# Kernel optimization log

Hardware: AMD Instinct MI355X
Metric: run time of the kernel (lower is better)

## Reference

```python
import jax, jax.numpy as jnp
import numpy as np

NUM_LAYERS = 2      # args.num_layers
EPS = 1e-6          # poincare_to_lorentz eps
NORM_CLIP = 1.0     # exp_map norm_control clip
N, K, F, D = 30000, 32, 256, 128


def _normalize_lorentz(h):
    # project onto hyperboloid: time = sqrt(1 + |space|^2)
    sp = h[:, 1:]
    t = jnp.sqrt(1.0 + jnp.sum(sp * sp, axis=-1, keepdims=True))
    return jnp.concatenate([t, sp], axis=-1)


def _exp_map_zero(v):
    # tangent vector at origin has zero time component (normalize_tan with x=0)
    sp = v[:, 1:]
    ldv = jnp.sum(sp * sp, axis=-1, keepdims=True)          # Lorentz norm^2 of (0, sp)
    nd = jnp.sqrt(jnp.clip(ldv + 1e-9, 1e-10, None))
    t = jnp.minimum(nd, NORM_CLIP)                           # norm_control
    time = jnp.cosh(t)
    space = jnp.sinh(t) * sp / nd
    return _normalize_lorentz(jnp.concatenate([time, space], axis=-1))


def _hyperbolic_mean(nbr, w):
    # nbr: [N, K, D] Lorentz points; w: [N, K] neighbor weights
    k = nbr[..., 1:] / nbr[..., :1]                          # h2k: Klein model
    kn = jnp.clip(jnp.sum(k * k, axis=-1, keepdims=True), 0.0, 0.9)
    lam = w[..., None] / jnp.sqrt(1.0 - kn)                  # weighted Lorentz factors
    k_mean = jnp.sum(lam * k, axis=1) / jnp.sum(lam, axis=1)  # [N, D-1]
    # k2h: Klein -> hyperboloid
    kn2 = jnp.minimum(jnp.sum(k_mean * k_mean, axis=-1, keepdims=True), 0.9)
    ones = jnp.ones((k_mean.shape[0], 1), k_mean.dtype)
    return jnp.concatenate([ones, k_mean], axis=-1) / jnp.sqrt(1.0 - kn2)


def _lorentz_activation(h):
    # lorentz -> poincare, SELU, poincare -> lorentz (c = 1)
    p = h[:, 1:] / (h[:, :1] + 1.0)
    p = jax.nn.selu(p)
    pn = jnp.sum(p * p, axis=-1, keepdims=True)
    return jnp.concatenate([1.0 + pn, 2.0 * p], axis=-1) / (1.0 - pn + EPS)


def setup_inputs() -> dict:
    key = jax.random.key(0)
    k1, k2, k3, k4, k5 = jax.random.split(key, 5)
    x = jax.random.normal(k1, (N, F), dtype=jnp.float32)
    adj = jax.random.randint(k2, (N, K), 0, N, dtype=jnp.int32)
    w = jax.random.uniform(k3, (N, K), dtype=jnp.float32)
    lin_W = jax.random.normal(k4, (F, D), dtype=jnp.float32) / np.sqrt(F)
    lin_b = jnp.zeros((D,), dtype=jnp.float32)
    M, _ = jnp.linalg.qr(jax.random.normal(k5, (D - 1, D - 1), dtype=jnp.float32))  # orthogonal init
    return {"x": x, "adj": adj, "w": w, "lin_W": lin_W, "lin_b": lin_b, "M": M}


def reference(x, adj, w, lin_W, lin_b, M):
    h = jax.nn.selu(x @ lin_W + lin_b)          # Euclidean projection + activation
    h = _exp_map_zero(h)                        # lift to hyperboloid
    d = h.shape[-1]
    # retrieve_params: block-diag [[1,0],[0,M]] Lorentz rotation (tie_weight -> shared)
    lw = jnp.zeros((d, d), h.dtype).at[0, 0].set(1.0).at[1:, 1:].set(M)
    for _ in range(NUM_LAYERS):
        msg = h @ lw                             # Stiefel transform
        nbr = msg[adj]                           # [N, K, D] neighbor gather
        h = _hyperbolic_mean(nbr, w)             # Klein weighted mean
        h = _lorentz_activation(h)               # SELU in Poincare model
        h = _normalize_lorentz(h)                # re-project onto hyperboloid
    return h
```

## Files before the change

### kernel.cpp

```cpp
#include <hip/hip_runtime.h>
#include <hip/hip_fp16.h>
#include <math.h>

#define NN 30000
#define KK 32
#define FF 256
#define DD 128
#define NB16 1875
#define SA 268

typedef _Float16 f16x8 __attribute__((ext_vector_type(8)));
typedef _Float16 f16x2 __attribute__((ext_vector_type(2)));
typedef float f32x4v __attribute__((ext_vector_type(4)));

__device__ __forceinline__ float seluf(float x) {
    const float scale = 1.0507009873554804934193349852946f;
    const float alpha = 1.6732632423543772848170429916717f;
    return x > 0.f ? scale * x : scale * alpha * expm1f(x);
}

__device__ __forceinline__ float waveReduceSum(float v) {
#pragma unroll
    for (int m = 1; m < 64; m <<= 1) v += __shfl_xor(v, m, 64);
    return v;
}

__global__ __launch_bounds__(256) void k_prep(
    const float* __restrict__ W, const float* __restrict__ M,
    _Float16* __restrict__ Wt, _Float16* __restrict__ Lt)
{
    const int b = blockIdx.x, t = threadIdx.x;
    if (b < 128) {
        Wt[b * FF + t] = (_Float16)W[t * DD + b];
    } else if (t < 128) {
        const int c = b - 128, k = t;
        const float v = (k == 0 && c == 0) ? 1.f
                      : ((k >= 1 && c >= 1) ? M[(k - 1) * 127 + (c - 1)] : 0.f);
        Lt[c * DD + k] = (_Float16)v;
    }
}

__global__ __launch_bounds__(256) void k_lin_exp_msg(
    const float* __restrict__ x, const _Float16* __restrict__ Wt,
    const float* __restrict__ b, const _Float16* __restrict__ Lt,
    __half* __restrict__ table)
{
    __shared__ _Float16 as_[16][SA];
    __shared__ _Float16 hhi[16][SA];
    __shared__ _Float16 hlo[16][SA];
    __shared__ float red[4][16];
    __shared__ float m0s[16];
    const int wv_ = threadIdx.x >> 6;
    const int lane = threadIdx.x & 63;
    const int g = lane >> 4, c16 = lane & 15;
    const int baseRow = blockIdx.x * 16;
    const int nb = wv_ * 2;
    const int arow = baseRow + c16;

    {
        const float4* xp = (const float4*)(x + (size_t)arow * FF);
#pragma unroll
        for (int i = 0; i < 2; ++i) {
            const int ks = wv_ * 2 + i;
            const float4 f0 = xp[ks * 8 + g * 2];
            const float4 f1 = xp[ks * 8 + g * 2 + 1];
            const float q[8] = {f0.x, f0.y, f0.z, f0.w, f1.x, f1.y, f1.z, f1.w};
            f16x8 a;
#pragma unroll
            for (int j = 0; j < 8; ++j) a[j] = (_Float16)q[j];
            *(f16x8*)&as_[c16][ks * 32 + g * 8] = a;
        }
    }
    __syncthreads();

    f16x8 bw0[8], bw1[8];
#pragma unroll
    for (int ks = 0; ks < 8; ++ks) {
        bw0[ks] = *(const f16x8*)(Wt + (size_t)((nb + 0) * 16 + c16) * FF + ks * 32 + g * 8);
        bw1[ks] = *(const f16x8*)(Wt + (size_t)((nb + 1) * 16 + c16) * FF + ks * 32 + g * 8);
    }
    f16x8 af[8];
#pragma unroll
    for (int ks = 0; ks < 8; ++ks)
        af[ks] = *(const f16x8*)&as_[c16][ks * 32 + g * 8];

    f32x4v acc[2];
    acc[0] = acc[1] = f32x4v{0.f, 0.f, 0.f, 0.f};
#pragma unroll
    for (int ks = 0; ks < 8; ++ks) {
        acc[0] = __builtin_amdgcn_mfma_f32_16x16x32_f16(af[ks], bw0[ks], acc[0], 0, 0, 0);
        acc[1] = __builtin_amdgcn_mfma_f32_16x16x32_f16(af[ks], bw1[ks], acc[1], 0, 0, 0);
    }

    float bias[2];
#pragma unroll
    for (int n = 0; n < 2; ++n) bias[n] = b[(nb + n) * 16 + c16];

    float vv[4][2];
#pragma unroll
    for (int r = 0; r < 4; ++r) {
        float part = 0.f;
#pragma unroll
        for (int n = 0; n < 2; ++n) {
            vv[r][n] = seluf(acc[n][r] + bias[n]);
            float sq = vv[r][n] * vv[r][n];
            if (wv_ == 0 && n == 0 && c16 == 0) sq = 0.f;
            part += sq;
        }
#pragma unroll
        for (int m = 1; m < 16; m <<= 1) part += __shfl_xor(part, m, 64);
        if (c16 == 0) red[wv_][4 * g + r] = part;
    }
    __syncthreads();
#pragma unroll
    for (int r = 0; r < 4; ++r) {
        const int lrow = 4 * g + r;
        const float ldv = red[0][lrow] + red[1][lrow] + red[2][lrow] + red[3][lrow];
        const float nd = sqrtf(fmaxf(ldv + 1e-9f, 1e-10f));
        const float t  = fminf(nd, 1.0f);
        const float sc = sinhf(t) / nd;
        const float tm = sqrtf(1.f + sc * sc * ldv);
#pragma unroll
        for (int n = 0; n < 2; ++n) {
            const int col = (nb + n) * 16 + c16;
            const float o = (wv_ == 0 && n == 0 && c16 == 0) ? tm : sc * vv[r][n];
            const _Float16 hi = (_Float16)o;
            hhi[lrow][col] = hi;
            hlo[lrow][col] = (_Float16)(o - (float)hi);
        }
    }
    __syncthreads();

    f16x8 bl0[4], bl1[4];
#pragma unroll
    for (int ks = 0; ks < 4; ++ks) {
        bl0[ks] = *(const f16x8*)(Lt + (size_t)((nb + 0) * 16 + c16) * DD + ks * 32 + g * 8);
        bl1[ks] = *(const f16x8*)(Lt + (size_t)((nb + 1) * 16 + c16) * DD + ks * 32 + g * 8);
    }
    f16x8 mh[4], ml[4];
#pragma unroll
    for (int ks = 0; ks < 4; ++ks) {
        mh[ks] = *(const f16x8*)&hhi[c16][ks * 32 + g * 8];
        ml[ks] = *(const f16x8*)&hlo[c16][ks * 32 + g * 8];
    }
    acc[0] = acc[1] = f32x4v{0.f, 0.f, 0.f, 0.f};
#pragma unroll
    for (int ks = 0; ks < 4; ++ks) {
        acc[0] = __builtin_amdgcn_mfma_f32_16x16x32_f16(mh[ks], bl0[ks], acc[0], 0, 0, 0);
        acc[0] = __builtin_amdgcn_mfma_f32_16x16x32_f16(ml[ks], bl0[ks], acc[0], 0, 0, 0);
        acc[1] = __builtin_amdgcn_mfma_f32_16x16x32_f16(mh[ks], bl1[ks], acc[1], 0, 0, 0);
        acc[1] = __builtin_amdgcn_mfma_f32_16x16x32_f16(ml[ks], bl1[ks], acc[1], 0, 0, 0);
    }

#pragma unroll
    for (int r = 0; r < 4; ++r) {
        float part = 0.f;
#pragma unroll
        for (int n = 0; n < 2; ++n) {
            float sq = acc[n][r] * acc[n][r];
            if (wv_ == 0 && n == 0 && c16 == 0) sq = 0.f;
            part += sq;
        }
#pragma unroll
        for (int m = 1; m < 16; m <<= 1) part += __shfl_xor(part, m, 64);
        if (c16 == 0) red[wv_][4 * g + r] = part;
        if (wv_ == 0 && c16 == 0) m0s[4 * g + r] = acc[0][r];
    }
    __syncthreads();
#pragma unroll
    for (int r = 0; r < 4; ++r) {
        const int lrow = 4 * g + r;
        const int row = baseRow + lrow;
        const float rn = 1.f / m0s[lrow];
        const float sum2 = red[0][lrow] + red[1][lrow] + red[2][lrow] + red[3][lrow];
        float kn = sum2 * rn * rn;
        kn = fminf(fmaxf(kn, 0.f), 0.9f);
        const float fh = 1.f / sqrtf(1.f - kn);
#pragma unroll
        for (int n = 0; n < 2; ++n) {
            const float val = (wv_ == 0 && n == 0 && c16 == 0) ? fh : acc[n][r] * rn;
            table[(size_t)row * DD + (nb + n) * 16 + c16] = __float2half(val);
        }
    }
}

__global__ __launch_bounds__(256) void k_layer_msg(
    const __half* __restrict__ tin, const int* __restrict__ adj,
    const float* __restrict__ w, const _Float16* __restrict__ Lt,
    __half* __restrict__ tout)
{
    __shared__ _Float16 hhi[16][SA];
    __shared__ _Float16 hlo[16][SA];
    __shared__ float red[4][16];
    __shared__ float m0s[16];
    const int wv_ = threadIdx.x >> 6;
    const int lane = threadIdx.x & 63;
    const int g = lane >> 4, c16 = lane & 15;
    const int baseNode = blockIdx.x * 16;

#pragma unroll
    for (int q = 0; q < 4; ++q) {
        const int node = baseNode + wv_ * 4 + q;
        const int   av = adj[node * KK + (lane & 31)];
        const float wvv = w[node * KK + (lane & 31)];

        unsigned int vbits[32];
#pragma unroll
        for (int j = 0; j < KK; ++j) {
            const int idx = __shfl(av, j, 64);
            vbits[j] = *(const unsigned int*)(tin + (size_t)idx * DD + lane * 2);
        }
        const float f = __half2float(tin[(size_t)av * DD]);
        const float lam = wvv * f;
        float ls = lam;
#pragma unroll
        for (int m = 1; m < 32; m <<= 1) ls += __shfl_xor(ls, m, 64);

        float km0 = 0.f, km1 = 0.f;
#pragma unroll
        for (int j = 0; j < KK; ++j) {
            const float cj = __shfl(lam, j, 64);
            const __half2 hh = *(const __half2*)&vbits[j];
            const float2 v = __half22float2(hh);
            km0 = fmaf(cj, v.x, km0);
            km1 = fmaf(cj, v.y, km1);
        }
        const float rl = 1.f / ls;
        const float m0 = km0 * rl;
        const float m1 = km1 * rl;
        float c2 = (lane ? m0 * m0 : 0.f) + m1 * m1;
        const float kn2 = fminf(waveReduceSum(c2), 0.9f);
        const float invs = 1.f / sqrtf(1.f - kn2);
        const float pd = invs + 1.f;
        const float p0 = lane ? seluf(m0 * invs / pd) : 0.f;
        const float p1 = seluf(m1 * invs / pd);
        float pc = p0 * p0 + p1 * p1;
        const float pn = waveReduceSum(pc);
        const float rdn = 1.f / (1.f - pn + 1e-6f);
        const float tm = sqrtf(1.f + 4.f * pn * rdn * rdn);
        const float ox = lane ? 2.f * p0 * rdn : tm;
        const float oy = 2.f * p1 * rdn;
        const int lrow = wv_ * 4 + q;
        const _Float16 hx = (_Float16)ox;
        const _Float16 hy = (_Float16)oy;
        f16x2 hi2, lo2;
        hi2[0] = hx; hi2[1] = hy;
        lo2[0] = (_Float16)(ox - (float)hx);
        lo2[1] = (_Float16)(oy - (float)hy);
        *(f16x2*)&hhi[lrow][2 * lane] = hi2;
        *(f16x2*)&hlo[lrow][2 * lane] = lo2;
    }
    __syncthreads();

    const int nb = wv_ * 2;
    f16x8 bl0[4], bl1[4];
#pragma unroll
    for (int ks = 0; ks < 4; ++ks) {
        bl0[ks] = *(const f16x8*)(Lt + (size_t)((nb + 0) * 16 + c16) * DD + ks * 32 + g * 8);
        bl1[ks] = *(const f16x8*)(Lt + (size_t)((nb + 1) * 16 + c16) * DD + ks * 32 + g * 8);
    }
    f16x8 mh[4], ml[4];
#pragma unroll
    for (int ks = 0; ks < 4; ++ks) {
        mh[ks] = *(const f16x8*)&hhi[c16][ks * 32 + g * 8];
        ml[ks] = *(const f16x8*)&hlo[c16][ks * 32 + g * 8];
    }
    f32x4v acc[2];
    acc[0] = acc[1] = f32x4v{0.f, 0.f, 0.f, 0.f};
#pragma unroll
    for (int ks = 0; ks < 4; ++ks) {
        acc[0] = __builtin_amdgcn_mfma_f32_16x16x32_f16(mh[ks], bl0[ks], acc[0], 0, 0, 0);
        acc[0] = __builtin_amdgcn_mfma_f32_16x16x32_f16(ml[ks], bl0[ks], acc[0], 0, 0, 0);
        acc[1] = __builtin_amdgcn_mfma_f32_16x16x32_f16(mh[ks], bl1[ks], acc[1], 0, 0, 0);
        acc[1] = __builtin_amdgcn_mfma_f32_16x16x32_f16(ml[ks], bl1[ks], acc[1], 0, 0, 0);
    }

#pragma unroll
    for (int r = 0; r < 4; ++r) {
        float part = 0.f;
#pragma unroll
        for (int n = 0; n < 2; ++n) {
            float sq = acc[n][r] * acc[n][r];
            if (wv_ == 0 && n == 0 && c16 == 0) sq = 0.f;
            part += sq;
        }
#pragma unroll
        for (int m = 1; m < 16; m <<= 1) part += __shfl_xor(part, m, 64);
        if (c16 == 0) red[wv_][4 * g + r] = part;
        if (wv_ == 0 && c16 == 0) m0s[4 * g + r] = acc[0][r];
    }
    __syncthreads();
#pragma unroll
    for (int r = 0; r < 4; ++r) {
        const int lrow = 4 * g + r;
        const int row = baseNode + lrow;
        const float rn = 1.f / m0s[lrow];
        const float sum2 = red[0][lrow] + red[1][lrow] + red[2][lrow] + red[3][lrow];
        float kn = sum2 * rn * rn;
        kn = fminf(fmaxf(kn, 0.f), 0.9f);
        const float fh = 1.f / sqrtf(1.f - kn);
#pragma unroll
        for (int n = 0; n < 2; ++n) {
            const float val = (wv_ == 0 && n == 0 && c16 == 0) ? fh : acc[n][r] * rn;
            tout[(size_t)row * DD + (nb + n) * 16 + c16] = __float2half(val);
        }
    }
}

__global__ __launch_bounds__(256) void k_layer(
    const __half* __restrict__ table, const int* __restrict__ adj,
    const float* __restrict__ w, float* __restrict__ out)
{
    const int wave = threadIdx.x >> 6;
    const int lane = threadIdx.x & 63;
    const int node = blockIdx.x * 4 + wave;

    const int   av = adj[node * KK + (lane & 31)];
    const float wv = w[node * KK + (lane & 31)];

    unsigned int vbits[32];
#pragma unroll
    for (int j = 0; j < KK; ++j) {
        const int idx = __shfl(av, j, 64);
        vbits[j] = *(const unsigned int*)(table + (size_t)idx * DD + lane * 2);
    }

    const float f  = __half2float(table[(size_t)av * DD]);
    const float lam = wv * f;
    float ls = lam;
#pragma unroll
    for (int m = 1; m < 32; m <<= 1) ls += __shfl_xor(ls, m, 64);

    float km0 = 0.f, km1 = 0.f;
#pragma unroll
    for (int j = 0; j < KK; ++j) {
        const float cj = __shfl(lam, j, 64);
        const __half2 hh = *(const __half2*)&vbits[j];
        const float2 v = __half22float2(hh);
        km0 = fmaf(cj, v.x, km0);
        km1 = fmaf(cj, v.y, km1);
    }
    const float rl = 1.f / ls;
    const float m0 = km0 * rl;
    const float m1 = km1 * rl;
    float c2 = (lane ? m0 * m0 : 0.f) + m1 * m1;
    const float kn2 = fminf(waveReduceSum(c2), 0.9f);
    const float invs = 1.f / sqrtf(1.f - kn2);
    const float pd = invs + 1.f;
    const float p0 = lane ? seluf(m0 * invs / pd) : 0.f;
    const float p1 = seluf(m1 * invs / pd);
    float pc = p0 * p0 + p1 * p1;
    const float pn = waveReduceSum(pc);
    const float rdn = 1.f / (1.f - pn + 1e-6f);
    const float tm = sqrtf(1.f + 4.f * pn * rdn * rdn);
    float2 o;
    o.x = lane ? 2.f * p0 * rdn : tm;
    o.y = 2.f * p1 * rdn;
    *(float2*)(out + (size_t)node * DD + lane * 2) = o;
}

extern "C" void kernel_launch(void* const* d_in, const int* in_sizes, int n_in,
                              void* d_out, int out_size, void* d_ws, size_t ws_size,
                              hipStream_t stream) {
    const float* x     = (const float*)d_in[0];
    const int*   adj   = (const int*)d_in[1];
    const float* w     = (const float*)d_in[2];
    const float* lin_W = (const float*)d_in[3];
    const float* lin_b = (const float*)d_in[4];
    const float* M     = (const float*)d_in[5];
    float*  out   = (float*)d_out;
    char*   ws    = (char*)d_ws;
    __half*   table0 = (__half*)ws;
    __half*   table1 = (__half*)(ws + 7680000);
    _Float16* Wt     = (_Float16*)(ws + 15360000);
    _Float16* Lt     = (_Float16*)(ws + 15425536);

    k_prep<<<256, 256, 0, stream>>>(lin_W, M, Wt, Lt);
    k_lin_exp_msg<<<NB16, 256, 0, stream>>>(x, Wt, lin_b, Lt, table0);
    k_layer_msg<<<NB16, 256, 0, stream>>>(table0, adj, w, Lt, table1);
    k_layer<<<NN / 4, 256, 0, stream>>>(table1, adj, w, out);
}
```

Measured before the change: 113.0 us.

## Use 16 waves per block in layer-msg kernel, one node per wave

The layer message kernel now launches 1024 threads per block, so each of 16 waves gathers and aggregates one node in parallel instead of four waves each looping over four nodes. The following small GEMM is split so 8 waves each compute one 16-column tile, with reductions widened to 8 partials. Separately, the first kernel reuses the hhi shared buffer for its input staging, which shrinks its LDS footprint. The aim is more memory-level parallelism on the gather and higher occupancy. The cost is half the waves idling during the GEMM phase and more register pressure under the new launch bounds.

```diff
diff --git a/kernel.cpp b/kernel.cpp
--- a/kernel.cpp
+++ b/kernel.cpp
@@ -45,7 +45,6 @@
     const float* __restrict__ b, const _Float16* __restrict__ Lt,
     __half* __restrict__ table)
 {
-    __shared__ _Float16 as_[16][SA];
     __shared__ _Float16 hhi[16][SA];
     __shared__ _Float16 hlo[16][SA];
     __shared__ float red[4][16];
@@ -68,7 +67,7 @@
             f16x8 a;
 #pragma unroll
             for (int j = 0; j < 8; ++j) a[j] = (_Float16)q[j];
-            *(f16x8*)&as_[c16][ks * 32 + g * 8] = a;
+            *(f16x8*)&hhi[c16][ks * 32 + g * 8] = a;
         }
     }
     __syncthreads();
@@ -82,7 +81,7 @@
     f16x8 af[8];
 #pragma unroll
     for (int ks = 0; ks < 8; ++ks)
-        af[ks] = *(const f16x8*)&as_[c16][ks * 32 + g * 8];
+        af[ks] = *(const f16x8*)&hhi[c16][ks * 32 + g * 8];
 
     f32x4v acc[2];
     acc[0] = acc[1] = f32x4v{0.f, 0.f, 0.f, 0.f};
@@ -184,23 +183,22 @@
     }
 }
 
-__global__ __launch_bounds__(256) void k_layer_msg(
+__global__ __launch_bounds__(1024, 8) void k_layer_msg(
     const __half* __restrict__ tin, const int* __restrict__ adj,
     const float* __restrict__ w, const _Float16* __restrict__ Lt,
     __half* __restrict__ tout)
 {
     __shared__ _Float16 hhi[16][SA];
     __shared__ _Float16 hlo[16][SA];
-    __shared__ float red[4][16];
+    __shared__ float red[8][16];
     __shared__ float m0s[16];
     const int wv_ = threadIdx.x >> 6;
     const int lane = threadIdx.x & 63;
     const int g = lane >> 4, c16 = lane & 15;
     const int baseNode = blockIdx.x * 16;
 
-#pragma unroll
-    for (int q = 0; q < 4; ++q) {
-        const int node = baseNode + wv_ * 4 + q;
+    {
+        const int node = baseNode + wv_;
         const int   av = adj[node * KK + (lane & 31)];
         const float wvv = w[node * KK + (lane & 31)];
 
@@ -240,69 +238,60 @@
         const float tm = sqrtf(1.f + 4.f * pn * rdn * rdn);
         const float ox = lane ? 2.f * p0 * rdn : tm;
         const float oy = 2.f * p1 * rdn;
-        const int lrow = wv_ * 4 + q;
         const _Float16 hx = (_Float16)ox;
         const _Float16 hy = (_Float16)oy;
         f16x2 hi2, lo2;
         hi2[0] = hx; hi2[1] = hy;
         lo2[0] = (_Float16)(ox - (float)hx);
         lo2[1] = (_Float16)(oy - (float)hy);
-        *(f16x2*)&hhi[lrow][2 * lane] = hi2;
-        *(f16x2*)&hlo[lrow][2 * lane] = lo2;
-    }
-    __syncthreads();
-
-    const int nb = wv_ * 2;
-    f16x8 bl0[4], bl1[4];
-#pragma unroll
-    for (int ks = 0; ks < 4; ++ks) {
-        bl0[ks] = *(const f16x8*)(Lt + (size_t)((nb + 0) * 16 + c16) * DD + ks * 32 + g * 8);
-        bl1[ks] = *(const f16x8*)(Lt + (size_t)((nb + 1) * 16 + c16) * DD + ks * 32 + g * 8);
-    }
-    f16x8 mh[4], ml[4];
-#pragma unroll
-    for (int ks = 0; ks < 4; ++ks) {
-        mh[ks] = *(const f16x8*)&hhi[c16][ks * 32 + g * 8];
-        ml[ks] = *(const f16x8*)&hlo[c16][ks * 32 + g * 8];
-    }
-    f32x4v acc[2];
-    acc[0] = acc[1] = f32x4v{0.f, 0.f, 0.f, 0.f};
-#pragma unroll
-    for (int ks = 0; ks < 4; ++ks) {
-        acc[0] = __builtin_amdgcn_mfma_f32_16x16x32_f16(mh[ks], bl0[ks], acc[0], 0, 0, 0);
-        acc[0] = __builtin_amdgcn_mfma_f32_16x16x32_f16(ml[ks], bl0[ks], acc[0], 0, 0, 0);
-        acc[1] = __builtin_amdgcn_mfma_f32_16x16x32_f16(mh[ks], bl1[ks], acc[1], 0, 0, 0);
-        acc[1] = __builtin_amdgcn_mfma_f32_16x16x32_f16(ml[ks], bl1[ks], acc[1], 0, 0, 0);
-    }
-
-#pragma unroll
-    for (int r = 0; r < 4; ++r) {
-        float part = 0.f;
-#pragma unroll
-        for (int n = 0; n < 2; ++n) {
-            float sq = acc[n][r] * acc[n][r];
-            if (wv_ == 0 && n == 0 && c16 == 0) sq = 0.f;
-            part += sq;
-        }
-#pragma unroll
-        for (int m = 1; m < 16; m <<= 1) part += __shfl_xor(part, m, 64);
-        if (c16 == 0) red[wv_][4 * g + r] = part;
-        if (wv_ == 0 && c16 == 0) m0s[4 * g + r] = acc[0][r];
-    }
-    __syncthreads();
-#pragma unroll
-    for (int r = 0; r < 4; ++r) {
-        const int lrow = 4 * g + r;
-        const int row = baseNode + lrow;
-        const float rn = 1.f / m0s[lrow];
-        const float sum2 = red[0][lrow] + red[1][lrow] + red[2][lrow] + red[3][lrow];
-        float kn = sum2 * rn * rn;
-        kn = fminf(fmaxf(kn, 0.f), 0.9f);
-        const float fh = 1.f / sqrtf(1.f - kn);
-#pragma unroll
-        for (int n = 0; n < 2; ++n) {
-            const float val = (wv_ == 0 && n == 0 && c16 == 0) ? fh : acc[n][r] * rn;
-            tout[(size_t)row * DD + (nb + n) * 16 + c16] = __float2half(val);
+        *(f16x2*)&hhi[wv_][2 * lane] = hi2;
+        *(f16x2*)&hlo[wv_][2 * lane] = lo2;
+    }
+    __syncthreads();
+
+    f32x4v acc = f32x4v{0.f, 0.f, 0.f, 0.f};
+    const int nb = wv_;
+    if (wv_ < 8) {
+        f16x8 bl[4];
+#pragma unroll
+        for (int ks = 0; ks < 4; ++ks)
+            bl[ks] = *(const f16x8*)(Lt + (size_t)(nb * 16 + c16) * DD + ks * 32 + g * 8);
+        f16x8 mh[4], ml[4];
+#pragma unroll
+        for (int ks = 0; ks < 4; ++ks) {
+            mh[ks] = *(const f16x8*)&hhi[c16][ks * 32 + g * 8];
+            ml[ks] = *(const f16x8*)&hlo[c16][ks * 32 + g * 8];
+        }
+#pragma unroll
+        for (int ks = 0; ks < 4; ++ks) {
+            acc = __builtin_amdgcn_mfma_f32_16x16x32_f16(mh[ks], bl[ks], acc, 0, 0, 0);
+            acc = __builtin_amdgcn_mfma_f32_16x16x32_f16(ml[ks], bl[ks], acc, 0, 0, 0);
+        }
+#pragma unroll
+        for (int r = 0; r < 4; ++r) {
+            float sq = acc[r] * acc[r];
+            if (nb == 0 && c16 == 0) sq = 0.f;
+#pragma unroll
+            for (int m = 1; m < 16; m <<= 1) sq += __shfl_xor(sq, m, 64);
+            if (c16 == 0) red[wv_][4 * g + r] = sq;
+            if (nb == 0 && c16 == 0) m0s[4 * g + r] = acc[r];
+        }
+    }
+    __syncthreads();
+    if (wv_ < 8) {
+#pragma unroll
+        for (int r = 0; r < 4; ++r) {
+            const int lrow = 4 * g + r;
+            const int row = baseNode + lrow;
+            const float rn = 1.f / m0s[lrow];
+            float sum2 = 0.f;
+#pragma unroll
+            for (int i = 0; i < 8; ++i) sum2 += red[i][lrow];
+            float kn = sum2 * rn * rn;
+            kn = fminf(fmaxf(kn, 0.f), 0.9f);
+            const float fh = 1.f / sqrtf(1.f - kn);
+            const float val = (nb == 0 && c16 == 0) ? fh : acc[r] * rn;
+            tout[(size_t)row * DD + nb * 16 + c16] = __float2half(val);
         }
     }
 }
@@ -377,6 +366,6 @@
 
     k_prep<<<256, 256, 0, stream>>>(lin_W, M, Wt, Lt);
     k_lin_exp_msg<<<NB16, 256, 0, stream>>>(x, Wt, lin_b, Lt, table0);
-    k_layer_msg<<<NB16, 256, 0, stream>>>(table0, adj, w, Lt, table1);
+    k_layer_msg<<<NB16, 1024, 0, stream>>>(table0, adj, w, Lt, table1);
     k_layer<<<NN / 4, 256, 0, stream>>>(table1, adj, w, out);
 }
```

Result: slower. 116.3 us (+2.9%).

## Split fused layer-1 gather and message kernel into two kernels via global scratch

Applied to the files above, without the earlier changes.

The fused layer kernel, in which each wave gathered four nodes sequentially and then ran a 16-row MFMA transform, is split in two. A one-node-per-wave gather/activation kernel writes hi/lo fp16 rows to global memory, reusing the output buffer as scratch, and a separate MFMA kernel applies the Lorentz rotation. The aim is more parallelism and memory-level overlap in the gather phase, which was serialized over four nodes per wave. The cost is an extra kernel launch and a global round-trip of about 15 MB. The first kernel also reuses the hhi shared array for the x tile, which reduces LDS use.

```diff
diff --git a/kernel.cpp b/kernel.cpp
--- a/kernel.cpp
+++ b/kernel.cpp
@@ -45,7 +45,6 @@
     const float* __restrict__ b, const _Float16* __restrict__ Lt,
     __half* __restrict__ table)
 {
-    __shared__ _Float16 as_[16][SA];
     __shared__ _Float16 hhi[16][SA];
     __shared__ _Float16 hlo[16][SA];
     __shared__ float red[4][16];
@@ -68,7 +67,7 @@
             f16x8 a;
 #pragma unroll
             for (int j = 0; j < 8; ++j) a[j] = (_Float16)q[j];
-            *(f16x8*)&as_[c16][ks * 32 + g * 8] = a;
+            *(f16x8*)&hhi[c16][ks * 32 + g * 8] = a;
         }
     }
     __syncthreads();
@@ -82,7 +81,7 @@
     f16x8 af[8];
 #pragma unroll
     for (int ks = 0; ks < 8; ++ks)
-        af[ks] = *(const f16x8*)&as_[c16][ks * 32 + g * 8];
+        af[ks] = *(const f16x8*)&hhi[c16][ks * 32 + g * 8];
 
     f32x4v acc[2];
     acc[0] = acc[1] = f32x4v{0.f, 0.f, 0.f, 0.f};
@@ -184,86 +183,89 @@
     }
 }
 
-__global__ __launch_bounds__(256) void k_layer_msg(
+__global__ __launch_bounds__(256) void k_layer_h(
     const __half* __restrict__ tin, const int* __restrict__ adj,
-    const float* __restrict__ w, const _Float16* __restrict__ Lt,
-    __half* __restrict__ tout)
-{
-    __shared__ _Float16 hhi[16][SA];
-    __shared__ _Float16 hlo[16][SA];
+    const float* __restrict__ w,
+    _Float16* __restrict__ hhi_g, _Float16* __restrict__ hlo_g)
+{
+    const int wave = threadIdx.x >> 6;
+    const int lane = threadIdx.x & 63;
+    const int node = blockIdx.x * 4 + wave;
+
+    const int   av = adj[node * KK + (lane & 31)];
+    const float wv = w[node * KK + (lane & 31)];
+
+    unsigned int vbits[32];
+#pragma unroll
+    for (int j = 0; j < KK; ++j) {
+        const int idx = __shfl(av, j, 64);
+        vbits[j] = *(const unsigned int*)(tin + (size_t)idx * DD + lane * 2);
+    }
+
+    const float f  = __half2float(tin[(size_t)av * DD]);
+    const float lam = wv * f;
+    float ls = lam;
+#pragma unroll
+    for (int m = 1; m < 32; m <<= 1) ls += __shfl_xor(ls, m, 64);
+
+    float km0 = 0.f, km1 = 0.f;
+#pragma unroll
+    for (int j = 0; j < KK; ++j) {
+        const float cj = __shfl(lam, j, 64);
+        const __half2 hh = *(const __half2*)&vbits[j];
+        const float2 v = __half22float2(hh);
+        km0 = fmaf(cj, v.x, km0);
+        km1 = fmaf(cj, v.y, km1);
+    }
+    const float rl = 1.f / ls;
+    const float m0 = km0 * rl;
+    const float m1 = km1 * rl;
+    float c2 = (lane ? m0 * m0 : 0.f) + m1 * m1;
+    const float kn2 = fminf(waveReduceSum(c2), 0.9f);
+    const float invs = 1.f / sqrtf(1.f - kn2);
+    const float pd = invs + 1.f;
+    const float p0 = lane ? seluf(m0 * invs / pd) : 0.f;
+    const float p1 = seluf(m1 * invs / pd);
+    float pc = p0 * p0 + p1 * p1;
+    const float pn = waveReduceSum(pc);
+    const float rdn = 1.f / (1.f - pn + 1e-6f);
+    const float tm = sqrtf(1.f + 4.f * pn * rdn * rdn);
+    const float ox = lane ? 2.f * p0 * rdn : tm;
+    const float oy = 2.f * p1 * rdn;
+    const _Float16 hx = (_Float16)ox;
+    const _Float16 hy = (_Float16)oy;
+    f16x2 hi2, lo2;
+    hi2[0] = hx; hi2[1] = hy;
+    lo2[0] = (_Float16)(ox - (float)hx);
+    lo2[1] = (_Float16)(oy - (float)hy);
+    *(f16x2*)&hhi_g[(size_t)node * DD + 2 * lane] = hi2;
+    *(f16x2*)&hlo_g[(size_t)node * DD + 2 * lane] = lo2;
+}
+
+__global__ __launch_bounds__(256) void k_msg(
+    const _Float16* __restrict__ hhi_g, const _Float16* __restrict__ hlo_g,
+    const _Float16* __restrict__ Lt, __half* __restrict__ tout)
+{
     __shared__ float red[4][16];
     __shared__ float m0s[16];
     const int wv_ = threadIdx.x >> 6;
     const int lane = threadIdx.x & 63;
     const int g = lane >> 4, c16 = lane & 15;
-    const int baseNode = blockIdx.x * 16;
-
-#pragma unroll
-    for (int q = 0; q < 4; ++q) {
-        const int node = baseNode + wv_ * 4 + q;
-        const int   av = adj[node * KK + (lane & 31)];
-        const float wvv = w[node * KK + (lane & 31)];
-
-        unsigned int vbits[32];
-#pragma unroll
-        for (int j = 0; j < KK; ++j) {
-            const int idx = __shfl(av, j, 64);
-            vbits[j] = *(const unsigned int*)(tin + (size_t)idx * DD + lane * 2);
-        }
-        const float f = __half2float(tin[(size_t)av * DD]);
-        const float lam = wvv * f;
-        float ls = lam;
-#pragma unroll
-        for (int m = 1; m < 32; m <<= 1) ls += __shfl_xor(ls, m, 64);
-
-        float km0 = 0.f, km1 = 0.f;
-#pragma unroll
-        for (int j = 0; j < KK; ++j) {
-            const float cj = __shfl(lam, j, 64);
-            const __half2 hh = *(const __half2*)&vbits[j];
-            const float2 v = __half22float2(hh);
-            km0 = fmaf(cj, v.x, km0);
-            km1 = fmaf(cj, v.y, km1);
-        }
-        const float rl = 1.f / ls;
-        const float m0 = km0 * rl;
-        const float m1 = km1 * rl;
-        float c2 = (lane ? m0 * m0 : 0.f) + m1 * m1;
-        const float kn2 = fminf(waveReduceSum(c2), 0.9f);
-        const float invs = 1.f / sqrtf(1.f - kn2);
-        const float pd = invs + 1.f;
-        const float p0 = lane ? seluf(m0 * invs / pd) : 0.f;
-        const float p1 = seluf(m1 * invs / pd);
-        float pc = p0 * p0 + p1 * p1;
-        const float pn = waveReduceSum(pc);
-        const float rdn = 1.f / (1.f - pn + 1e-6f);
-        const float tm = sqrtf(1.f + 4.f * pn * rdn * rdn);
-        const float ox = lane ? 2.f * p0 * rdn : tm;
-        const float oy = 2.f * p1 * rdn;
-        const int lrow = wv_ * 4 + q;
-        const _Float16 hx = (_Float16)ox;
-        const _Float16 hy = (_Float16)oy;
-        f16x2 hi2, lo2;
-        hi2[0] = hx; hi2[1] = hy;
-        lo2[0] = (_Float16)(ox - (float)hx);
-        lo2[1] = (_Float16)(oy - (float)hy);
-        *(f16x2*)&hhi[lrow][2 * lane] = hi2;
-        *(f16x2*)&hlo[lrow][2 * lane] = lo2;
-    }
-    __syncthreads();
-
+    const int baseRow = blockIdx.x * 16;
     const int nb = wv_ * 2;
+    const int arow = baseRow + c16;
+
+    f16x8 mh[4], ml[4];
+#pragma unroll
+    for (int ks = 0; ks < 4; ++ks) {
+        mh[ks] = *(const f16x8*)(hhi_g + (size_t)arow * DD + ks * 32 + g * 8);
+        ml[ks] = *(const f16x8*)(hlo_g + (size_t)arow * DD + ks * 32 + g * 8);
+    }
     f16x8 bl0[4], bl1[4];
 #pragma unroll
     for (int ks = 0; ks < 4; ++ks) {
         bl0[ks] = *(const f16x8*)(Lt + (size_t)((nb + 0) * 16 + c16) * DD + ks * 32 + g * 8);
         bl1[ks] = *(const f16x8*)(Lt + (size_t)((nb + 1) * 16 + c16) * DD + ks * 32 + g * 8);
-    }
-    f16x8 mh[4], ml[4];
-#pragma unroll
-    for (int ks = 0; ks < 4; ++ks) {
-        mh[ks] = *(const f16x8*)&hhi[c16][ks * 32 + g * 8];
-        ml[ks] = *(const f16x8*)&hlo[c16][ks * 32 + g * 8];
     }
     f32x4v acc[2];
     acc[0] = acc[1] = f32x4v{0.f, 0.f, 0.f, 0.f};
@@ -293,7 +295,7 @@
 #pragma unroll
     for (int r = 0; r < 4; ++r) {
         const int lrow = 4 * g + r;
-        const int row = baseNode + lrow;
+        const int row = baseRow + lrow;
         const float rn = 1.f / m0s[lrow];
         const float sum2 = red[0][lrow] + red[1][lrow] + red[2][lrow] + red[3][lrow];
         float kn = sum2 * rn * rn;
@@ -374,9 +376,12 @@
     __half*   table1 = (__half*)(ws + 7680000);
     _Float16* Wt     = (_Float16*)(ws + 15360000);
     _Float16* Lt     = (_Float16*)(ws + 15425536);
+    _Float16* hhi_g  = (_Float16*)d_out;
+    _Float16* hlo_g  = (_Float16*)((char*)d_out + 7680000);
 
     k_prep<<<256, 256, 0, stream>>>(lin_W, M, Wt, Lt);
     k_lin_exp_msg<<<NB16, 256, 0, stream>>>(x, Wt, lin_b, Lt, table0);
-    k_layer_msg<<<NB16, 256, 0, stream>>>(table0, adj, w, Lt, table1);
+    k_layer_h<<<NN / 4, 256, 0, stream>>>(table0, adj, w, hhi_g, hlo_g);
+    k_msg<<<NB16, 256, 0, stream>>>(hhi_g, hlo_g, Lt, table1);
     k_layer<<<NN / 4, 256, 0, stream>>>(table1, adj, w, out);
 }
```

Result: slower. 119.4 us (+5.6%).
